# Performance work log

Hardware: AMD Instinct MI355X
Metric: run time of the kernel (lower is better)

Reference implementation:

```python
import jax, jax.numpy as jnp
import numpy as np

B, T, H, M, R, W = 32, 64, 512, 128, 4, 64
EPS = 1e-6  # cosine-similarity delta


def setup_inputs() -> dict:
    key = jax.random.key(0)
    ks = jax.random.split(key, 6)
    s = 0.05
    isz = R * W + H          # 768: controller / mem_out input size
    xi = W * R + 3 * W + 5 * R + 3  # 471: memory interface size
    return {
        "x": jax.random.normal(ks[0], (B, T, H), jnp.float32),
        "W_ih": jax.random.normal(ks[1], (4 * H, isz), jnp.float32) * s,
        "W_hh": jax.random.normal(ks[2], (4 * H, H), jnp.float32) * s,
        "b_ih": jnp.zeros((4 * H,), jnp.float32),
        "b_hh": jnp.zeros((4 * H,), jnp.float32),
        "W_xi": jax.random.normal(ks[3], (xi, H), jnp.float32) * s,
        "b_xi": jnp.zeros((xi,), jnp.float32),
        "W_o": jax.random.normal(ks[4], (H, isz), jnp.float32) * s,
        "b_o": jnp.zeros((H,), jnp.float32),
    }


def _cosine(mem, keys):
    # mem (B,M,W), keys (B,K,W) -> (B,K,M)
    dot = jnp.einsum('bkw,bmw->bkm', keys, mem)
    nk = jnp.linalg.norm(keys, axis=-1)[:, :, None]
    nm = jnp.linalg.norm(mem, axis=-1)[:, None, :]
    return dot / (nk * nm + EPS)


def _dnc_forward(x, W_ih, W_hh, b_ih, b_hh, W_xi, b_xi, W_o, b_o):
    eye = jnp.eye(M, dtype=x.dtype)
    splits = list(np.cumsum([R * W, R, W, 1, W, W, R, 1, 1]))

    def step(carry, x_t):
        h, c, mem, link, prec, rw, ww, usage, last_read = carry
        # ---- LSTM controller cell ----
        inp = jnp.concatenate([x_t, last_read], -1)           # (B, 768)
        gates = inp @ W_ih.T + b_ih + h @ W_hh.T + b_hh
        i_g, f_g, g_g, o_g = jnp.split(gates, 4, axis=-1)
        c = jax.nn.sigmoid(f_g) * c + jax.nn.sigmoid(i_g) * jnp.tanh(g_g)
        h = jax.nn.sigmoid(o_g) * jnp.tanh(c)

        # ---- interface vector ----
        xi = h @ W_xi.T + b_xi
        rk, rs, wk, ws, ev, wv, fg, ag, wg, rm = jnp.split(xi, splits, axis=-1)
        read_keys = jnp.tanh(rk.reshape(-1, R, W))            # (B,R,W)
        read_str = jax.nn.softplus(rs)                        # (B,R)
        write_key = jnp.tanh(wk)[:, None, :]                  # (B,1,W)
        write_str = jax.nn.softplus(ws)                       # (B,1)
        erase = jax.nn.sigmoid(ev)                            # (B,W)
        write_vec = jnp.tanh(wv)                              # (B,W)
        free_g = jax.nn.sigmoid(fg)                           # (B,R)
        alloc_g = jax.nn.sigmoid(ag)                          # (B,1)
        write_g = jax.nn.sigmoid(wg)                          # (B,1)
        read_modes = jax.nn.softmax(rm.reshape(-1, R, 3), -1)

        # ---- usage vector ----
        usage = usage + (1.0 - usage) * ww                    # single write head
        psi = jnp.prod(1.0 - free_g[:, :, None] * rw, axis=1)
        usage = usage * psi

        # ---- write content weighting ----
        wcw = jax.nn.softmax(_cosine(mem, write_key)[:, 0, :] * write_str, axis=-1)

        # ---- allocation weighting (sort + shifted cumprod) ----
        u = 5e-6 + (1.0 - 5e-6) * usage
        phi = jnp.argsort(u, axis=1)                          # ascending usage
        su = jnp.take_along_axis(u, phi, 1)
        shifted = jnp.cumprod(
            jnp.concatenate([jnp.ones_like(su[:, :1]), su], 1), axis=1)[:, :-1]
        sa = (1.0 - su) * shifted
        alloc = jnp.take_along_axis(sa, jnp.argsort(phi, axis=1), 1)

        # ---- write weighting ----
        ww = write_g * (alloc_g * alloc + (1.0 - alloc_g) * wcw)  # (B,M)

        # ---- erase + write memory ----
        mem = mem * (1.0 - ww[:, :, None] * erase[:, None, :]) \
            + ww[:, :, None] * write_vec[:, None, :]

        # ---- temporal link matrix + precedence ----
        link = (1.0 - ww[:, :, None] - ww[:, None, :]) * link \
            + ww[:, :, None] * prec[:, None, :]
        link = link * (1.0 - eye)
        prec = (1.0 - jnp.sum(ww, -1, keepdims=True)) * prec + ww

        # ---- read weighting (content + forward + backward modes) ----
        ccw = jax.nn.softmax(_cosine(mem, read_keys) * read_str[:, :, None], axis=-1)
        fwd = jnp.einsum('bij,brj->bri', link, rw)
        bwd = jnp.einsum('bri,bij->brj', rw, link)
        rw = read_modes[:, :, 0:1] * bwd + read_modes[:, :, 1:2] * fwd \
            + read_modes[:, :, 2:3] * ccw
        read_vecs = jnp.einsum('brm,bmw->brw', rw, mem)
        last_read = read_vecs.reshape(-1, R * W)

        out = jnp.concatenate([h, last_read], -1) @ W_o.T + b_o
        return (h, c, mem, link, prec, rw, ww, usage, last_read), out

    b = x.shape[0]
    z = lambda *s: jnp.zeros(s, x.dtype)
    carry0 = (z(b, H), z(b, H), jnp.full((b, M, W), EPS, x.dtype),
              z(b, M, M), z(b, M), z(b, R, M), z(b, M), z(b, M), z(b, R * W))
    _, outs = jax.lax.scan(step, carry0, jnp.swapaxes(x, 0, 1))
    return jnp.swapaxes(outs, 0, 1)  # (B, T, H)


def reference(x, W_ih, W_hh, b_ih, b_hh, W_xi, b_xi, W_o, b_o):
    return _dnc_forward(x, W_ih, W_hh, b_ih, b_hh, W_xi, b_xi, W_o, b_o)
```

## Files before the change

### kernel.cpp

```cpp
#include <hip/hip_runtime.h>
#include <math.h>

#define TPB 1024
#define NBLK 160
#define NBATCH 32
#define NT 64
#define NH 512
#define NM 128
#define NR 4
#define NW 64
#define NI 768
#define NXI 471
#define EPSF 1e-6f
#define MS 68
#define MS4 17
#define LKS 129


typedef float f4 __attribute__((ext_vector_type(4)));

#define WS_PUBH  0
#define WS_PUBRV (WS_PUBH + 2*NBATCH*NH)
#define WS_PUBXI (WS_PUBRV + 2*NBATCH*NR*NW)
#define WS_FLAGS (WS_PUBXI + 2*NBATCH*480)
#define D_G 0
#define D_R 128
#define D_X 160
#define D_TOTAL 288
#define NXB 118

__device__ __forceinline__ float sigm(float x){ return 1.0f/(1.0f+expf(-x)); }
__device__ __forceinline__ float sftp(float x){ return fmaxf(x,0.0f)+log1pf(expf(-fabsf(x))); }
__device__ __forceinline__ float dot4(f4 a, f4 b){
    return a.x*b.x + a.y*b.y + a.z*b.z + a.w*b.w;
}
__device__ __forceinline__ float wave_red(float v){
    #pragma unroll
    for (int o = 32; o > 0; o >>= 1) v += __shfl_down(v, o);
    return v;
}

__device__ __forceinline__ f4 cload4(const float* p){
    f4 v;
    asm volatile("global_load_dwordx4 %0, %1, off sc0 sc1\n\t"
                 "s_waitcnt vmcnt(0)"
                 : "=&v"(v) : "v"(p) : "memory");
    return v;
}
__device__ __forceinline__ void cload4x2(const float* p0, const float* p1,
                                         f4& a, f4& b){
    asm volatile("global_load_dwordx4 %0, %2, off sc0 sc1\n\t"
                 "global_load_dwordx4 %1, %3, off sc0 sc1\n\t"
                 "s_waitcnt vmcnt(0)"
                 : "=&v"(a), "=&v"(b) : "v"(p0), "v"(p1) : "memory");
}
__device__ __forceinline__ void cload4x4(const float* p0, const float* p1,
                                         const float* p2, const float* p3,
                                         f4& a, f4& b, f4& c, f4& d){
    asm volatile("global_load_dwordx4 %0, %4, off sc0 sc1\n\t"
                 "global_load_dwordx4 %1, %5, off sc0 sc1\n\t"
                 "global_load_dwordx4 %2, %6, off sc0 sc1\n\t"
                 "global_load_dwordx4 %3, %7, off sc0 sc1\n\t"
                 "s_waitcnt vmcnt(0)"
                 : "=&v"(a), "=&v"(b), "=&v"(c), "=&v"(d)
                 : "v"(p0), "v"(p1), "v"(p2), "v"(p3) : "memory");
}
__device__ __forceinline__ void cstore4(float* p, f4 v){
    asm volatile("global_store_dwordx4 %0, %1, off sc0 sc1"
                 :: "v"(p), "v"(v) : "memory");
}
__device__ __forceinline__ void cstore1(float* p, float v){
    asm volatile("global_store_dword %0, %1, off sc0 sc1"
                 :: "v"(p), "v"(v) : "memory");
}

__device__ __forceinline__ void multi_wait_d(const unsigned int* f, int n,
                                             unsigned int tgt, int tid){
    if (tid < n) {
        const unsigned int* p = f + tid;
        while (__hip_atomic_load(p, __ATOMIC_RELAXED,
                                 __HIP_MEMORY_SCOPE_AGENT) < tgt)
            __builtin_amdgcn_s_sleep(2);
    }
    __syncthreads();
}
__device__ __forceinline__ void flag_set_d(unsigned int* f, unsigned int v, int tid){
    asm volatile("s_waitcnt vmcnt(0)" ::: "memory");
    __syncthreads();
    if (tid == 0)
        __hip_atomic_store(f, v, __ATOMIC_RELAXED, __HIP_MEMORY_SCOPE_AGENT);
}

__global__ void dnc_zero(float* ws){
    unsigned int* z = (unsigned int*)(ws + WS_FLAGS);
    for (int e = threadIdx.x; e < D_TOTAL; e += blockDim.x) z[e] = 0u;
}

#define O_MEM 0
#define O_RW2 8704
#define O_WW2 9728
#define O_USG 9984
#define O_PRC 10112
#define O_XI  10240
#define O_KEY 10720
#define O_WK  10976
#define O_ER  11040
#define O_WV  11104
#define O_RS  11168
#define O_FG  11172
#define O_MD  11176
#define O_NK  11188
#define O_SC  11192
#define O_NRM 11200
#define O_WCW 11456
#define O_UU  11584
#define O_SU  11712
#define O_CUM 11840
#define O_RNK 11968
#define O_CCW 12096
#define O_RED 12608
#define O_PF  12624
#define O_PB  16720
#define O_PK  12624
#define O_LK  20816
#define S_SZ  (20816 + NM*LKS)
#define G_ACC 8192
#define G_C   8736
#define G_H   8896

__global__ __launch_bounds__(TPB) void dnc_pipe2(
    const float* __restrict__ x, const float* __restrict__ W_ih,
    const float* __restrict__ W_hh, const float* __restrict__ b_ih,
    const float* __restrict__ b_hh, const float* __restrict__ W_xi,
    const float* __restrict__ b_xi, const float* __restrict__ W_o,
    const float* __restrict__ b_o, float* __restrict__ out,
    float* __restrict__ ws)
{
    __shared__ __align__(16) float S[S_SZ];

    const int tid = threadIdx.x;
    const int wv  = tid >> 6;
    const int l   = tid & 63;
    const int bid = blockIdx.x;

    float* __restrict__ pubH  = ws + WS_PUBH;
    float* __restrict__ pubRV = ws + WS_PUBRV;
    float* __restrict__ pubXI = ws + WS_PUBXI;
    unsigned int* __restrict__ FLGD = (unsigned int*)(ws + WS_FLAGS);

    if (bid < NBATCH) {
        const int b = bid;
        float* lk = S+O_LK;
        float* mem = S+O_MEM;
        float* usg = S+O_USG;  float* prc = S+O_PRC; float* xiS = S+O_XI;
        float* keys = S+O_KEY; float* wkey = S+O_WK; float* ers = S+O_ER;
        float* wvec = S+O_WV;  float* rstr = S+O_RS; float* fgte = S+O_FG;
        float* modes = S+O_MD; float* nkey = S+O_NK; float* sc = S+O_SC;
        float* nrm = S+O_NRM;  float* wcw = S+O_WCW;
        float* uu = S+O_UU;    float* su = S+O_SU;   float* cum = S+O_CUM;
        int*   rnk = (int*)(S+O_RNK);
        float* ccw = S+O_CCW;  float* red = S+O_RED;

        for (int e = tid; e < NM*LKS; e += TPB) lk[e] = 0.0f;
        for (int e = tid; e < NM*NW; e += TPB) mem[(e>>6)*MS + (e&63)] = EPSF;
        for (int e = tid; e < 2*NR*NM; e += TPB) S[O_RW2+e]=0.0f;
        for (int e = tid; e < 2*NM; e += TPB) S[O_WW2+e]=0.0f;
        for (int e = tid; e < NM; e += TPB){ usg[e]=0.0f; prc[e]=0.0f; }
        for (int e = tid; e < 2*NM; e += TPB) nrm[e] = 8.0f*EPSF;
        __syncthreads();

        for (int t = 0; t < NT; ++t) {
            const int par = t & 1;
            float* nmo = nrm + 128*par;
            float* nmn = nrm + 128*(par^1);
            float* rwC = S + O_RW2 + 512*par;
            float* rwN = S + O_RW2 + 512*(par^1);
            float* wwP = S + O_WW2 + 128*(par^1);
            float* wwC = S + O_WW2 + 128*par;

            multi_wait_d(&FLGD[D_X], NXB, (unsigned)(t+1), tid);
            if (tid < 120)
                *(f4*)&xiS[tid*4] =
                    cload4(&pubXI[(size_t)par*NBATCH*480 + b*480 + tid*4]);
            __syncthreads();

            if (tid < 256)       keys[tid] = tanhf(xiS[tid]);
            else if (tid < 260)  rstr[tid-256] = sftp(xiS[tid]);
            else if (tid < 324)  wkey[tid-260] = tanhf(xiS[tid]);
            else if (tid == 324) sc[0] = sftp(xiS[324]);
            else if (tid < 389)  ers[tid-325] = sigm(xiS[tid]);
            else if (tid < 453)  wvec[tid-389] = tanhf(xiS[tid]);
            else if (tid < 457)  fgte[tid-453] = sigm(xiS[tid]);
            else if (tid == 457) sc[1] = sigm(xiS[457]);
            else if (tid == 458) sc[2] = sigm(xiS[458]);
            else if (tid < 463) {
                int r = tid - 459;
                float a0=xiS[459+3*r], a1=xiS[460+3*r], a2=xiS[461+3*r];
                float mx = fmaxf(a0, fmaxf(a1, a2));
                float e0=expf(a0-mx), e1=expf(a1-mx), e2=expf(a2-mx);
                float si = 1.0f/(e0+e1+e2);
                modes[3*r]=e0*si; modes[3*r+1]=e1*si; modes[3*r+2]=e2*si;
            }
            __syncthreads();

            if (wv < 4) {
                float v = keys[wv*NW + l];
                float s2 = wave_red(v*v);
                if (l == 0) nkey[wv] = sqrtf(s2);
            } else if (wv == 4) {
                float v = wkey[l];
                float s2 = wave_red(v*v);
                if (l == 0) sc[3] = sqrtf(s2);
            } else if (wv == 6 || wv == 7) {
                int m = tid - 384;
                float u = usg[m];
                u = u + (1.0f - u)*wwP[m];
                float psi = 1.0f;
                #pragma unroll
                for (int r = 0; r < NR; ++r) psi *= (1.0f - fgte[r]*rwC[r*NM+m]);
                u *= psi;
                usg[m] = u;
                uu[m] = 5e-6f + (1.0f - 5e-6f)*u;
            }
            __syncthreads();

            {
                const int m = tid >> 3, s = tid & 7;
                const f4* mem4 = (const f4*)(S + O_MEM);
                const f4* wk4  = (const f4*)(S + O_WK);
                f4 m0 = mem4[m*MS4 + s*2], m1 = mem4[m*MS4 + s*2 + 1];
                f4 k0 = wk4[s*2], k1 = wk4[s*2 + 1];
                float d = dot4(m0, k0) + dot4(m1, k1);
                d += __shfl_down(d, 4); d += __shfl_down(d, 2); d += __shfl_down(d, 1);
                if (s == 0) wcw[m] = d/(sc[3]*nmo[m] + EPSF) * sc[0];
            }
            __syncthreads();

            if (tid < 64) {
                float w0 = wcw[l], w1 = wcw[l+64];
                float mx = fmaxf(w0, w1);
                #pragma unroll
                for (int o = 32; o > 0; o >>= 1) mx = fmaxf(mx, __shfl_down(mx, o));
                float M = __shfl(mx, 0);
                float e0 = expf(w0 - M), e1 = expf(w1 - M);
                float s = wave_red(e0 + e1);
                float inv = 1.0f/__shfl(s, 0);
                wcw[l] = e0*inv; wcw[l+64] = e1*inv;
            } else if (tid >= 512) {
                const int q = tid - 512, m = q >> 2, s = q & 3;
                const float um = uu[m];
                int rk = 0;
                #pragma unroll 8
                for (int k = 0; k < 32; ++k) {
                    int j = 4*k + s;
                    float uj = uu[j];
                    rk += (uj < um) || (uj == um && j < m);
                }
                rk += __shfl_down(rk, 1); rk += __shfl_down(rk, 2);
                if (s == 0) { rnk[m] = rk; su[rk] = um; }
            }
            __syncthreads();

            if (tid < 64) {
                float a = su[tid], bb = su[64+tid];
                #pragma unroll
                for (int o = 1; o < 64; o <<= 1) {
                    float ta = __shfl_up(a, o);
                    float tb = __shfl_up(bb, o);
                    if (tid >= o) { a *= ta; bb *= tb; }
                }
                float P0 = __shfl(a, 63);
                cum[tid] = a;
                cum[64+tid] = P0*bb;
            }
            __syncthreads();

            if (tid < NM) {
                int rk = rnk[tid];
                float excl = (rk == 0) ? 1.0f : cum[rk-1];
                float al = (1.0f - uu[tid])*excl;
                wwC[tid] = sc[2]*(sc[1]*al + (1.0f - sc[1])*wcw[tid]);
                float sal = wave_red(al);
                if (l == 0) red[2 + wv] = sal;
            }
            __syncthreads();

            if (tid == 1023)
                sc[4] = sc[2]*(sc[1]*(red[2]+red[3]) + (1.0f - sc[1]));
            #pragma unroll
            for (int ri = 0; ri < 8; ++ri) {
                int row = wv*8 + ri;
                float wm = wwC[row];
                float v = mem[row*MS + l];
                float nv = v*(1.0f - wm*ers[l]) + wm*wvec[l];
                mem[row*MS + l] = nv;
                float s2 = wave_red(nv*nv);
                if (l == 0) nmn[row] = sqrtf(s2);
            }
            __syncthreads();

            if (tid < 512) {
                const int m = tid >> 2, s = tid & 3;
                const f4* mem4 = (const f4*)(S + O_MEM);
                const f4* key4 = (const f4*)(S + O_KEY);
                float a0=0.f, a1=0.f, a2=0.f, a3=0.f;
                #pragma unroll
                for (int c = 0; c < 4; ++c) {
                    f4 mv = mem4[m*MS4 + s*4 + c];
                    f4 k0 = key4[0*16 + s*4 + c];
                    f4 k1 = key4[1*16 + s*4 + c];
                    f4 k2 = key4[2*16 + s*4 + c];
                    f4 k3 = key4[3*16 + s*4 + c];
                    a0 += dot4(mv, k0); a1 += dot4(mv, k1);
                    a2 += dot4(mv, k2); a3 += dot4(mv, k3);
                }
                a0 += __shfl_down(a0,1); a0 += __shfl_down(a0,2);
                a1 += __shfl_down(a1,1); a1 += __shfl_down(a1,2);
                a2 += __shfl_down(a2,1); a2 += __shfl_down(a2,2);
                a3 += __shfl_down(a3,1); a3 += __shfl_down(a3,2);
                if (s == 0) {
                    float nm = nmn[m];
                    ccw[0*NM+m] = a0/(nkey[0]*nm + EPSF)*rstr[0];
                    ccw[1*NM+m] = a1/(nkey[1]*nm + EPSF)*rstr[1];
                    ccw[2*NM+m] = a2/(nkey[2]*nm + EPSF)*rstr[2];
                    ccw[3*NM+m] = a3/(nkey[3]*nm + EPSF)*rstr[3];
                }
            } else {
                const int wj = wv - 8;
                const int i0 = wj*16;
                const float wmA = wwC[l], wmB = wwC[64+l];
                float fA0=0,fA1=0,fA2=0,fA3=0, fB0=0,fB1=0,fB2=0,fB3=0;
                #pragma unroll 4
                for (int ii = 0; ii < 16; ++ii) {
                    const int i = i0 + ii;
                    float pri = prc[i];
                    float wwi = wwC[i];
                    float r0 = rwC[0*NM+i];
                    float r1 = rwC[1*NM+i];
                    float r2 = rwC[2*NM+i];
                    float r3 = rwC[3*NM+i];
                    float lrA = lk[l*LKS + i];
                    float nA = (i == l) ? 0.0f
                             : (1.0f - wmA - wwi)*lrA + wmA*pri;
                    lk[l*LKS + i] = nA;
                    float lrB = lk[(l+64)*LKS + i];
                    float nB = (i == l+64) ? 0.0f
                             : (1.0f - wmB - wwi)*lrB + wmB*pri;
                    lk[(l+64)*LKS + i] = nB;
                    fA0 += nA*r0; fA1 += nA*r1; fA2 += nA*r2; fA3 += nA*r3;
                    fB0 += nB*r0; fB1 += nB*r1; fB2 += nB*r2; fB3 += nB*r3;
                }
                float* Pf = S + O_PF + wj*512;
                Pf[0*NM+l]=fA0; Pf[1*NM+l]=fA1; Pf[2*NM+l]=fA2; Pf[3*NM+l]=fA3;
                Pf[0*NM+64+l]=fB0; Pf[1*NM+64+l]=fB1;
                Pf[2*NM+64+l]=fB2; Pf[3*NM+64+l]=fB3;
            }
            __syncthreads();

            if (tid < 256) {
                float v0 = ccw[wv*NM + l], v1 = ccw[wv*NM + 64 + l];
                float mx = fmaxf(v0, v1);
                #pragma unroll
                for (int o = 32; o > 0; o >>= 1) mx = fmaxf(mx, __shfl_down(mx, o));
                float M = __shfl(mx, 0);
                float e0 = expf(v0 - M), e1 = expf(v1 - M);
                float s = wave_red(e0 + e1);
                float inv = 1.0f/__shfl(s, 0);
                ccw[wv*NM + l] = e0*inv; ccw[wv*NM + 64 + l] = e1*inv;
            } else if (tid < 384) {
                int m = tid - 256;
                prc[m] = (1.0f - sc[4])*prc[m] + wwC[m];
            } else if (wv >= 8) {
                const int wj = wv - 8;
                const int i0 = wj*16;
                float bA0=0,bA1=0,bA2=0,bA3=0, bB0=0,bB1=0,bB2=0,bB3=0;
                #pragma unroll 4
                for (int ii = 0; ii < 16; ++ii) {
                    const int i = i0 + ii;
                    float r0 = rwC[0*NM+i];
                    float r1 = rwC[1*NM+i];
                    float r2 = rwC[2*NM+i];
                    float r3 = rwC[3*NM+i];
                    float lcA = lk[i*LKS + l];
                    float lcB = lk[i*LKS + 64 + l];
                    bA0 += lcA*r0; bA1 += lcA*r1; bA2 += lcA*r2; bA3 += lcA*r3;
                    bB0 += lcB*r0; bB1 += lcB*r1; bB2 += lcB*r2; bB3 += lcB*r3;
                }
                float* Pb = S + O_PB + wj*512;
                Pb[0*NM+l]=bA0; Pb[1*NM+l]=bA1; Pb[2*NM+l]=bA2; Pb[3*NM+l]=bA3;
                Pb[0*NM+64+l]=bB0; Pb[1*NM+64+l]=bB1;
                Pb[2*NM+64+l]=bB2; Pb[3*NM+64+l]=bB3;
            }
            __syncthreads();

            if (tid < 512) {
                const int r = tid >> 7, m = tid & 127;
                float fs = 0.0f, bs = 0.0f;
                #pragma unroll
                for (int c = 0; c < 8; ++c) {
                    fs += S[O_PF + c*512 + r*NM + m];
                    bs += S[O_PB + c*512 + r*NM + m];
                }
                rwN[r*NM + m] = modes[3*r]*bs + modes[3*r+1]*fs
                              + modes[3*r+2]*ccw[r*NM + m];
            }
            __syncthreads();

            if (wv < 8) {
                const int m0 = wv*16;
                float a0=0.f, a1=0.f, a2=0.f, a3=0.f;
                #pragma unroll 4
                for (int mm = 0; mm < 16; ++mm) {
                    const int m = m0 + mm;
                    float rn0 = rwN[0*NM + m];
                    float rn1 = rwN[1*NM + m];
                    float rn2 = rwN[2*NM + m];
                    float rn3 = rwN[3*NM + m];
                    float mv = mem[m*MS + l];
                    a0 += rn0*mv; a1 += rn1*mv; a2 += rn2*mv; a3 += rn3*mv;
                }
                float* Pk = S + O_PK + wv*256;
                Pk[0*64+l]=a0; Pk[1*64+l]=a1; Pk[2*64+l]=a2; Pk[3*64+l]=a3;
            }
            __syncthreads();

            if (tid < 256) {
                const int r = tid >> 6, w = tid & 63;
                float s = 0.0f;
                #pragma unroll
                for (int c = 0; c < 8; ++c) s += S[O_PK + c*256 + r*64 + w];
                cstore1(&pubRV[(size_t)par*NBATCH*NR*NW + b*NR*NW + r*NW + w], s);
            }
            flag_set_d(&FLGD[D_R + b], (unsigned)(t+1), tid);
        }
    } else {
        const int g = bid - 32;
        const int gate = wv >> 2, j = wv & 3;
        const int r = gate*NH + 4*g + j;
        const f4* WA = (const f4*)(W_ih + (size_t)r*NI);
        f4 wx0 = WA[l], wx1 = WA[l+64], wrv = WA[128+l];
        const f4* WB = (const f4*)(W_hh + (size_t)r*NH);
        f4 wh0 = WB[l], wh1 = WB[l+64];
        const float bias = b_ih[r] + b_hh[r];
        float* accS = S + G_ACC;
        float* cSg  = S + G_C;
        float* hStg = S + G_H;
        const int sbi = tid >> 7, sk4 = (tid & 127) << 2;

        if (tid < 160) cSg[tid] = 0.0f;
        for (int e = tid; e < NBATCH*NH; e += TPB) hStg[e] = 0.0f;
        __syncthreads();

        for (int t = 0; t <= NT; ++t) {
            const int par = t & 1, parp = (t+1) & 1;

            if (t >= 1) {
                multi_wait_d(&FLGD[D_G], 128, (unsigned)t, tid);
                const float* hIn = pubH + (size_t)parp*NBATCH*NH;
                f4 a0, a1, a2, a3;
                cload4x4(hIn + tid*4, hIn + (tid+1024)*4,
                         hIn + (tid+2048)*4, hIn + (tid+3072)*4,
                         a0, a1, a2, a3);
                *(f4*)&hStg[tid*4]          = a0;
                *(f4*)&hStg[(tid+1024)*4]   = a1;
                *(f4*)&hStg[(tid+2048)*4]   = a2;
                *(f4*)&hStg[(tid+3072)*4]   = a3;
                __syncthreads();
                if (g < NXB) {
                    float* xOut = pubXI + (size_t)parp*NBATCH*480;
                    #pragma unroll
                    for (int bb = 0; bb < 2; ++bb) {
                        const int bi = 2*wv + bb;
                        const f4* H4 = (const f4*)(hStg + bi*512);
                        f4 res = {0.0f, 0.0f, 0.0f, 0.0f};
                        #pragma unroll
                        for (int jj = 0; jj < 4; ++jj) {
                            const int row = 4*g + jj;
                            if (row < NXI) {
                                const f4* WX = (const f4*)(W_xi + (size_t)row*NH);
                                float a = dot4(WX[l], H4[l])
                                        + dot4(WX[l+64], H4[l+64]);
                                a = wave_red(a);
                                res[jj] = a + b_xi[row];
                            }
                        }
                        if (l == 0) cstore4(&xOut[(size_t)bi*480 + 4*g], res);
                    }
                    flag_set_d(&FLGD[D_X + g], (unsigned)t, tid);
                }
            }

            if (t < NT) {
                for (int p = 0; p < 4; ++p) {
                    const int b0 = p*8;
                    *(f4*)&S[sbi*512 + sk4] =
                        *(const f4*)&x[((size_t)(b0+sbi)*NT + t)*NH + sk4];
                    __syncthreads();
                    #pragma unroll
                    for (int bi = 0; bi < 8; ++bi) {
                        const f4* X4 = (const f4*)(S + bi*512);
                        const f4* H4 = (const f4*)(hStg + (b0+bi)*512);
                        float a = dot4(wx0, X4[l]) + dot4(wx1, X4[l+64])
                                + dot4(wh0, H4[l]) + dot4(wh1, H4[l+64]);
                        a = wave_red(a);
                        if (l == 0) accS[(b0+bi)*17 + wv] = a + bias;
                    }
                    __syncthreads();
                }
            }

            {
                const int bi0 = tid >> 6, k40 = (tid & 63) << 2;
                if (t >= 1) {
                    multi_wait_d(&FLGD[D_R], 32, (unsigned)t, tid);
                    const float* rIn = pubRV + (size_t)parp*NBATCH*NR*NW;
                    f4 a0, a1;
                    cload4x2(&rIn[bi0*256 + k40], &rIn[(bi0+16)*256 + k40], a0, a1);
                    *(f4*)&S[bi0*256 + k40] = a0;
                    *(f4*)&S[(bi0+16)*256 + k40] = a1;
                } else {
                    f4 z = {0.0f, 0.0f, 0.0f, 0.0f};
                    *(f4*)&S[bi0*256 + k40] = z;
                    *(f4*)&S[(bi0+16)*256 + k40] = z;
                }
            }
            __syncthreads();

            if (t < NT) {
                #pragma unroll
                for (int bi = 0; bi < 32; ++bi) {
                    const f4* RV4 = (const f4*)(S + bi*256);
                    float d = dot4(wrv, RV4[l]);
                    d = wave_red(d);
                    if (l == 0) accS[bi*17 + wv] += d;
                }
                __syncthreads();
                if (tid < 32) {
                    const int bi = tid;
                    const float* acc = accS + bi*17;
                    f4 hq;
                    #pragma unroll
                    for (int jj = 0; jj < 4; ++jj) {
                        float i_ = sigm(acc[0*4 + jj]);
                        float f_ = sigm(acc[1*4 + jj]);
                        float g_ = tanhf(acc[2*4 + jj]);
                        float o_ = sigm(acc[3*4 + jj]);
                        float c  = f_*cSg[bi*5 + jj] + i_*g_;
                        cSg[bi*5 + jj] = c;
                        hq[jj] = o_*tanhf(c);
                    }
                    cstore4(&pubH[(size_t)par*NBATCH*NH + (size_t)bi*NH + 4*g], hq);
                }
                flag_set_d(&FLGD[D_G + g], (unsigned)(t+1), tid);
            }

            if (t >= 1) {
                #pragma unroll
                for (int bb = 0; bb < 2; ++bb) {
                    const int bi = 2*wv + bb;
                    const f4* H4 = (const f4*)(hStg + bi*512);
                    const f4* RV4 = (const f4*)(S + bi*256);
                    f4 res;
                    #pragma unroll
                    for (int jj = 0; jj < 4; ++jj) {
                        const int row = 4*g + jj;
                        const f4* WO = (const f4*)(W_o + (size_t)row*NI);
                        float a = dot4(WO[l], H4[l]) + dot4(WO[l+64], H4[l+64])
                                + dot4(WO[128+l], RV4[l]);
                        a = wave_red(a);
                        res[jj] = a + b_o[row];
                    }
                    if (l == 0)
                        *(f4*)&out[((size_t)bi*NT + (t-1))*NH + 4*g] = res;
                }
            }
        }
    }
}

extern "C" void kernel_launch(void* const* d_in, const int* in_sizes, int n_in,
                              void* d_out, int out_size, void* d_ws, size_t ws_size,
                              hipStream_t stream) {
    (void)in_sizes; (void)n_in; (void)out_size; (void)ws_size;
    const float* x    = (const float*)d_in[0];
    const float* W_ih = (const float*)d_in[1];
    const float* W_hh = (const float*)d_in[2];
    const float* b_ih = (const float*)d_in[3];
    const float* b_hh = (const float*)d_in[4];
    const float* W_xi = (const float*)d_in[5];
    const float* b_xi = (const float*)d_in[6];
    const float* W_o  = (const float*)d_in[7];
    const float* b_o  = (const float*)d_in[8];
    float* out = (float*)d_out;
    float* ws  = (float*)d_ws;

    dnc_zero<<<1, 512, 0, stream>>>(ws);

    void* args[] = { (void*)&x, (void*)&W_ih, (void*)&W_hh, (void*)&b_ih,
                     (void*)&b_hh, (void*)&W_xi, (void*)&b_xi, (void*)&W_o,
                     (void*)&b_o, (void*)&out, (void*)&ws };
    hipLaunchCooperativeKernel((void*)dnc_pipe2, dim3(NBLK), dim3(TPB),
                               args, 0, stream);
}
```

Baseline: 2.625 ms.

## Precompute output H-projection early, load interface directly, vectorize memory norms

Three changes. Batch blocks now load interface values straight from global memory into their activation functions, dropping the shared staging buffer and one barrier; the read-mode softmax gathers its inputs with wave shuffles. The memory-norm computation becomes a separate vectorized pass using 8-lane partial reductions instead of a full wave reduction per row. Gate blocks compute the h-part of the output projection before they wait for read vectors, which leaves only the read-vector part on the critical path after the wait, at the cost of extra shared memory and a special case for the final step.

```diff
diff --git a/kernel.cpp b/kernel.cpp
--- a/kernel.cpp
+++ b/kernel.cpp
@@ -47,6 +47,13 @@
                  : "=&v"(v) : "v"(p) : "memory");
     return v;
 }
+__device__ __forceinline__ float cload1f(const float* p){
+    float v;
+    asm volatile("global_load_dword %0, %1, off sc0 sc1\n\t"
+                 "s_waitcnt vmcnt(0)"
+                 : "=&v"(v) : "v"(p) : "memory");
+    return v;
+}
 __device__ __forceinline__ void cload4x2(const float* p0, const float* p1,
                                          f4& a, f4& b){
     asm volatile("global_load_dwordx4 %0, %2, off sc0 sc1\n\t"
@@ -101,7 +108,6 @@
 #define O_WW2 9728
 #define O_USG 9984
 #define O_PRC 10112
-#define O_XI  10240
 #define O_KEY 10720
 #define O_WK  10976
 #define O_ER  11040
@@ -127,6 +133,7 @@
 #define G_ACC 8192
 #define G_C   8736
 #define G_H   8896
+#define G_OH  25280
 
 __global__ __launch_bounds__(TPB) void dnc_pipe2(
     const float* __restrict__ x, const float* __restrict__ W_ih,
@@ -152,7 +159,7 @@
         const int b = bid;
         float* lk = S+O_LK;
         float* mem = S+O_MEM;
-        float* usg = S+O_USG;  float* prc = S+O_PRC; float* xiS = S+O_XI;
+        float* usg = S+O_USG;  float* prc = S+O_PRC;
         float* keys = S+O_KEY; float* wkey = S+O_WK; float* ers = S+O_ER;
         float* wvec = S+O_WV;  float* rstr = S+O_RS; float* fgte = S+O_FG;
         float* modes = S+O_MD; float* nkey = S+O_NK; float* sc = S+O_SC;
@@ -179,27 +186,30 @@
             float* wwC = S + O_WW2 + 128*par;
 
             multi_wait_d(&FLGD[D_X], NXB, (unsigned)(t+1), tid);
-            if (tid < 120)
-                *(f4*)&xiS[tid*4] =
-                    cload4(&pubXI[(size_t)par*NBATCH*480 + b*480 + tid*4]);
-            __syncthreads();
-
-            if (tid < 256)       keys[tid] = tanhf(xiS[tid]);
-            else if (tid < 260)  rstr[tid-256] = sftp(xiS[tid]);
-            else if (tid < 324)  wkey[tid-260] = tanhf(xiS[tid]);
-            else if (tid == 324) sc[0] = sftp(xiS[324]);
-            else if (tid < 389)  ers[tid-325] = sigm(xiS[tid]);
-            else if (tid < 453)  wvec[tid-389] = tanhf(xiS[tid]);
-            else if (tid < 457)  fgte[tid-453] = sigm(xiS[tid]);
-            else if (tid == 457) sc[1] = sigm(xiS[457]);
-            else if (tid == 458) sc[2] = sigm(xiS[458]);
-            else if (tid < 463) {
-                int r = tid - 459;
-                float a0=xiS[459+3*r], a1=xiS[460+3*r], a2=xiS[461+3*r];
-                float mx = fmaxf(a0, fmaxf(a1, a2));
-                float e0=expf(a0-mx), e1=expf(a1-mx), e2=expf(a2-mx);
-                float si = 1.0f/(e0+e1+e2);
-                modes[3*r]=e0*si; modes[3*r+1]=e1*si; modes[3*r+2]=e2*si;
+            {
+                const float* xb = pubXI + (size_t)par*NBATCH*480 + b*480;
+                if (tid < 256)       keys[tid] = tanhf(cload1f(xb+tid));
+                else if (tid < 260)  rstr[tid-256] = sftp(cload1f(xb+tid));
+                else if (tid < 324)  wkey[tid-260] = tanhf(cload1f(xb+tid));
+                else if (tid == 324) sc[0] = sftp(cload1f(xb+324));
+                else if (tid < 389)  ers[tid-325] = sigm(cload1f(xb+tid));
+                else if (tid < 453)  wvec[tid-389] = tanhf(cload1f(xb+tid));
+                else if (tid < 457)  fgte[tid-453] = sigm(cload1f(xb+tid));
+                else if (tid == 457) sc[1] = sigm(cload1f(xb+457));
+                else if (tid == 458) sc[2] = sigm(cload1f(xb+458));
+                else if (tid < 471) {
+                    float xv = cload1f(xb + tid);
+                    int r = tid - 459;
+                    float a0 = __shfl(xv, 11 + 3*r);
+                    float a1 = __shfl(xv, 12 + 3*r);
+                    float a2 = __shfl(xv, 13 + 3*r);
+                    if (r < 4) {
+                        float mx = fmaxf(a0, fmaxf(a1, a2));
+                        float e0=expf(a0-mx), e1=expf(a1-mx), e2=expf(a2-mx);
+                        float si = 1.0f/(e0+e1+e2);
+                        modes[3*r]=e0*si; modes[3*r+1]=e1*si; modes[3*r+2]=e2*si;
+                    }
+                }
             }
             __syncthreads();
 
@@ -292,10 +302,17 @@
                 int row = wv*8 + ri;
                 float wm = wwC[row];
                 float v = mem[row*MS + l];
-                float nv = v*(1.0f - wm*ers[l]) + wm*wvec[l];
-                mem[row*MS + l] = nv;
-                float s2 = wave_red(nv*nv);
-                if (l == 0) nmn[row] = sqrtf(s2);
+                mem[row*MS + l] = v*(1.0f - wm*ers[l]) + wm*wvec[l];
+            }
+            {
+                const int row = wv*8 + (l>>3);
+                const f4* mem4 = (const f4*)(S + O_MEM);
+                f4 m0 = mem4[row*MS4 + (l&7)*2];
+                f4 m1 = mem4[row*MS4 + (l&7)*2 + 1];
+                float s2 = dot4(m0,m0) + dot4(m1,m1);
+                s2 += __shfl_down(s2, 4); s2 += __shfl_down(s2, 2);
+                s2 += __shfl_down(s2, 1);
+                if ((l & 7) == 0) nmn[row] = sqrtf(s2);
             }
             __syncthreads();
 
@@ -445,6 +462,7 @@
         float* accS = S + G_ACC;
         float* cSg  = S + G_C;
         float* hStg = S + G_H;
+        float* oH   = S + G_OH;
         const int sbi = tid >> 7, sk4 = (tid & 127) << 2;
 
         if (tid < 160) cSg[tid] = 0.0f;
@@ -507,6 +525,19 @@
                     }
                     __syncthreads();
                 }
+                #pragma unroll
+                for (int bb = 0; bb < 2; ++bb) {
+                    const int bi = 2*wv + bb;
+                    const f4* H4 = (const f4*)(hStg + bi*512);
+                    #pragma unroll
+                    for (int jj = 0; jj < 4; ++jj) {
+                        const int row = 4*g + jj;
+                        const f4* WO = (const f4*)(W_o + (size_t)row*NI);
+                        float a = dot4(WO[l], H4[l]) + dot4(WO[l+64], H4[l+64]);
+                        a = wave_red(a);
+                        if (l == 0) oH[bi*5 + jj] = a;
+                    }
+                }
             }
 
             {
@@ -565,10 +596,15 @@
                     for (int jj = 0; jj < 4; ++jj) {
                         const int row = 4*g + jj;
                         const f4* WO = (const f4*)(W_o + (size_t)row*NI);
-                        float a = dot4(WO[l], H4[l]) + dot4(WO[l+64], H4[l+64])
-                                + dot4(WO[128+l], RV4[l]);
+                        float a = dot4(WO[128+l], RV4[l]);
+                        if (t == NT) {
+                            a += dot4(WO[l], H4[l]) + dot4(WO[l+64], H4[l+64]);
+                        }
                         a = wave_red(a);
-                        res[jj] = a + b_o[row];
+                        if (l == 0) {
+                            float hp = (t < NT) ? oH[bi*5 + jj] : 0.0f;
+                            res[jj] = a + hp + b_o[row];
+                        }
                     }
                     if (l == 0)
                         *(f4*)&out[((size_t)bi*NT + (t-1))*NH + 4*g] = res;
```

Result: faster. 2.565 ms (-2.3%).
